# Kernel optimization log

Measured on AMD Instinct MI355X. Metric: run time of the kernel, lower is better.

## Reference

```python
import jax, jax.numpy as jnp
import numpy as np

D, H, W = 16, 16, 16          # token grid = img_size/patch_size at i_layer=0
NUM_HEADS = 8
DISTANCE = 10.0               # 10 - i_layer


def _local_pattern(d, h, w, distance):
    # faithful to local_nd_pattern: meshgrid (ij), flatten, cdist p=2, < distance
    g = jnp.meshgrid(jnp.arange(d), jnp.arange(h), jnp.arange(w), indexing='ij')
    coords = jnp.stack([c.reshape(-1) for c in g], axis=1).astype(jnp.float32)  # [N,3]
    diff = coords[:, None, :] - coords[None, :, :]                               # [N,N,3]
    dist = jnp.sqrt(jnp.sum(diff * diff, axis=-1))
    return dist < distance                                                       # [N,N] bool


def setup_inputs() -> dict:
    key = jax.random.key(0)
    k1, k2, k3 = jax.random.split(key, 3)
    dim = 256
    x = jax.random.normal(k1, (1, dim, D, H, W), dtype=jnp.float32)
    qkv_w = jax.random.normal(k2, (3 * dim, dim), dtype=jnp.float32) * (dim ** -0.5)
    proj_w = jax.random.normal(k3, (dim, dim), dtype=jnp.float32) * (dim ** -0.5)
    proj_b = jnp.zeros((dim,), dtype=jnp.float32)
    return {"x": x, "qkv_w": qkv_w, "proj_w": proj_w, "proj_b": proj_b}


def reference(x, qkv_w, proj_w, proj_b):
    b, c, d, h, w = x.shape
    n = d * h * w
    hd = c // NUM_HEADS
    mask = _local_pattern(d, h, w, DISTANCE)                  # [N,N] bool

    # b c d h w -> b (dhw) c
    tok = x.reshape(b, c, n).transpose(0, 2, 1)               # [B,N,C]
    qkv = jnp.einsum('bnc,oc->bno', tok, qkv_w)               # [B,N,3C]
    qkv = qkv.reshape(b, n, 3, NUM_HEADS, hd)
    qkv = qkv.transpose(2, 0, 3, 1, 4)                        # [3,B,H,N,hd]
    q, k, v = qkv[0], qkv[1], qkv[2]                          # [B,H,N,hd]

    scale = 1.0 / jnp.sqrt(jnp.asarray(hd, dtype=x.dtype))
    scores = jnp.einsum('bhnd,bhmd->bhnm', q, k) * scale      # [B,H,N,N]
    scores = jnp.where(mask[None, None], scores, -jnp.inf)
    attn = jax.nn.softmax(scores, axis=-1)
    out = jnp.einsum('bhnm,bhmd->bhnd', attn, v)              # [B,H,N,hd]

    out = out.transpose(0, 2, 1, 3).reshape(b, n, c)          # [B,N,C]
    out = jnp.einsum('bnc,oc->bno', out, proj_w) + proj_b
    # b (dhw) c -> b c d h w
    out = out.transpose(0, 2, 1).reshape(b, c, d, h, w)
    return out
```

## Files before the change

### kernel.cpp

```cpp
#include <hip/hip_runtime.h>
#include <hip/hip_bf16.h>

typedef __attribute__((ext_vector_type(8))) short short8;
typedef __attribute__((ext_vector_type(4))) float floatx4;

#define L2E 1.4426950408889634f

#if __has_builtin(__builtin_amdgcn_exp2f)
#define EXP2(x) __builtin_amdgcn_exp2f(x)
#else
#define EXP2(x) exp2f(x)
#endif
#if __has_builtin(__builtin_amdgcn_rcpf)
#define RCP(x) __builtin_amdgcn_rcpf(x)
#else
#define RCP(x) (1.0f / (x))
#endif

static __device__ __forceinline__ unsigned short f2bf(float f) {
    unsigned int u = __builtin_bit_cast(unsigned int, f);
    u += 0x7fffu + ((u >> 16) & 1u);
    return (unsigned short)(u >> 16);
}
static __device__ __forceinline__ unsigned int pk_bf16(float a, float b) {
    __hip_bfloat162 h2 = __float22bfloat162_rn(make_float2(a, b));
    unsigned int u;
    __builtin_memcpy(&u, &h2, 4);
    return u;
}

__global__ __launch_bounds__(256) void k_qkv(const float* __restrict__ x,
                                             const float* __restrict__ qw,
                                             unsigned short* __restrict__ qm,
                                             unsigned short* __restrict__ km,
                                             unsigned short* __restrict__ vt) {
    __shared__ __align__(16) unsigned short At[64][136];
    __shared__ __align__(16) unsigned short Wt[64][136];
    const int tid = threadIdx.x;
    const int wave = tid >> 6, lane = tid & 63;
    const int l16 = lane & 15, quad = lane >> 4;
    const int m0 = blockIdx.x * 64;
    const int o0 = blockIdx.y * 64;

    floatx4 acc[4] = {};
    for (int rnd = 0; rnd < 2; ++rnd) {
        const int cbase = rnd * 128;
        if (rnd) __syncthreads();
        {
            const int tok0 = (tid & 15) * 4;
            const int c0   = (tid >> 4) * 8;
            const float* xp = x + (size_t)(cbase + c0) * 4096 + m0 + tok0;
            float4 v[8];
            #pragma unroll
            for (int j = 0; j < 8; ++j)
                v[j] = *reinterpret_cast<const float4*>(xp + (size_t)j * 4096);
            #pragma unroll
            for (int t = 0; t < 4; ++t) {
                unsigned int d[4];
                d[0] = pk_bf16((&v[0].x)[t], (&v[1].x)[t]);
                d[1] = pk_bf16((&v[2].x)[t], (&v[3].x)[t]);
                d[2] = pk_bf16((&v[4].x)[t], (&v[5].x)[t]);
                d[3] = pk_bf16((&v[6].x)[t], (&v[7].x)[t]);
                __builtin_memcpy(&At[tok0 + t][c0], d, 16);
            }
        }
        {
            const int o_l = tid >> 2, cp = (tid & 3) * 32;
            const float4* wp = reinterpret_cast<const float4*>(
                qw + (size_t)(o0 + o_l) * 256 + cbase + cp);
            #pragma unroll
            for (int j = 0; j < 2; ++j) {
                const float4 g0 = wp[4 * j + 0], g1 = wp[4 * j + 1];
                const float4 g2 = wp[4 * j + 2], g3 = wp[4 * j + 3];
                unsigned int u[8];
                u[0] = pk_bf16(g0.x, g0.y); u[1] = pk_bf16(g0.z, g0.w);
                u[2] = pk_bf16(g1.x, g1.y); u[3] = pk_bf16(g1.z, g1.w);
                u[4] = pk_bf16(g2.x, g2.y); u[5] = pk_bf16(g2.z, g2.w);
                u[6] = pk_bf16(g3.x, g3.y); u[7] = pk_bf16(g3.z, g3.w);
                __builtin_memcpy(&Wt[o_l][cp + 16 * j], u, 32);
            }
        }
        __syncthreads();
        #pragma unroll
        for (int cc = 0; cc < 4; ++cc) {
            const int c0 = cc * 32 + quad * 8;
            const short8 a = *reinterpret_cast<const short8*>(&At[wave * 16 + l16][c0]);
            #pragma unroll
            for (int t4 = 0; t4 < 4; ++t4) {
                const short8 b = *reinterpret_cast<const short8*>(&Wt[t4 * 16 + l16][c0]);
                acc[t4] = __builtin_amdgcn_mfma_f32_16x16x32_bf16(a, b, acc[t4], 0, 0, 0);
            }
        }
    }

    const int s = o0 >> 8;
    if (s < 2) {
        const float qscale = 0.17677669529663687f * L2E;
        #pragma unroll
        for (int t4 = 0; t4 < 4; ++t4) {
            #pragma unroll
            for (int r = 0; r < 4; ++r) {
                const int n = m0 + wave * 16 + quad * 4 + r;
                const int o = o0 + t4 * 16 + l16;
                const int rem = o & 255, head = rem >> 5, t = rem & 31;
                if (s == 0)  qm[((size_t)head * 4096 + n) * 32 + t] = f2bf(acc[t4][r] * qscale);
                else         km[((size_t)head * 4096 + n) * 32 + t] = f2bf(acc[t4][r]);
            }
        }
    } else {
        __syncthreads();
        unsigned short (*Ct)[72] = reinterpret_cast<unsigned short(*)[72]>(&At[0][0]);
        #pragma unroll
        for (int t4 = 0; t4 < 4; ++t4) {
            unsigned int d2[2];
            d2[0] = pk_bf16(acc[t4][0], acc[t4][1]);
            d2[1] = pk_bf16(acc[t4][2], acc[t4][3]);
            __builtin_memcpy(&Ct[t4 * 16 + l16][wave * 16 + quad * 4], d2, 8);
        }
        __syncthreads();
        const int row = tid >> 2, col0 = (tid & 3) * 16;
        unsigned short* dst = vt + (size_t)(o0 - 512 + row) * 4096 + m0 + col0;
        const short8 ca = *reinterpret_cast<const short8*>(&Ct[row][col0]);
        const short8 cb = *reinterpret_cast<const short8*>(&Ct[row][col0 + 8]);
        *reinterpret_cast<short8*>(dst) = ca;
        *reinterpret_cast<short8*>(dst + 8) = cb;
    }
}

__global__ __launch_bounds__(256, 2) void k_attn(const unsigned short* __restrict__ qm,
                                                 const unsigned short* __restrict__ km,
                                                 const unsigned short* __restrict__ vt,
                                                 unsigned short* __restrict__ ao) {
    const int h   = blockIdx.y;
    const int nq0 = blockIdx.x * 64;
    const int tid = threadIdx.x;
    const int wv  = tid >> 6;
    const int lane = tid & 63;
    const int l16 = lane & 15, quad = lane >> 4;
    const int nqw = nq0 + wv * 16;

    __shared__ __align__(16) unsigned short Kt[2][2][2048];
    __shared__ __align__(16) unsigned short Vt[2][2][2048];
    __shared__ __align__(16) unsigned short PT[4][2][16][72];

    const short8 a_q = *reinterpret_cast<const short8*>(
        qm + ((size_t)h * 4096 + nqw + l16) * 32 + quad * 8);

    const int hq = (nqw >> 4) & 15;
    const int dq = nq0 >> 8;
    float dw2[4];
    #pragma unroll
    for (int r = 0; r < 4; ++r) {
        const float dw = (float)(quad * 4 + r - l16);
        dw2[r] = dw * dw;
    }

    const int dk_lo = (dq > 9) ? dq - 9 : 0;
    const int dk_hi = (dq < 6) ? dq + 9 : 15;
    const int NT = 4 * (dk_hi - dk_lo + 1);

    const int skey = tid >> 2;
    const int sdo  = (tid & 3) * 8;
    const int sdim = tid >> 3;
    const int skg  = tid & 7;
    const unsigned short* ksrc = km + ((size_t)h << 17) + skey * 32 + sdo;
    const unsigned short* vsrc = vt + (((size_t)h * 32 + sdim) << 12) + skg * 8;
    const int kdst = (skey * 32 + sdo) ^ ((skey & 7) << 3);
    const int vdst = (skg * 256 + sdim * 8) ^ (skg << 3);

    float l_acc = 0.f;
    floatx4 o_acc[2][2] = {};

#define J0T(T) (((dk_lo + ((T) >> 2)) << 8) + (((T) & 3) << 6))

    short8 rK[2], rV[2];
#define LOAD2(TA, TB) {                                                   \
        const int ja_ = J0T(TA), jb_ = J0T(TB);                           \
        rK[0] = *reinterpret_cast<const short8*>(ksrc + (size_t)ja_ * 32);\
        rV[0] = *reinterpret_cast<const short8*>(vsrc + ja_);             \
        rK[1] = *reinterpret_cast<const short8*>(ksrc + (size_t)jb_ * 32);\
        rV[1] = *reinterpret_cast<const short8*>(vsrc + jb_);             \
    }
#define WRITE2(NB) {                                                      \
        *reinterpret_cast<short8*>(&Kt[NB][0][kdst]) = rK[0];             \
        *reinterpret_cast<short8*>(&Vt[NB][0][vdst]) = rV[0];             \
        *reinterpret_cast<short8*>(&Kt[NB][1][kdst]) = rK[1];             \
        *reinterpret_cast<short8*>(&Vt[NB][1][vdst]) = rV[1];             \
    }

#define THR(T, TH) {                                                      \
        const int dk_ = dk_lo + ((T) >> 2), g_ = (T) & 3;                 \
        const int dd_ = dq - dk_;                                         \
        const int bb_ = 100 - dd_ * dd_;                                  \
        const int h0_ = hq - 4 * g_;                                      \
        TH[0] = bb_ - h0_ * h0_;                                          \
        TH[1] = bb_ - (h0_ - 1) * (h0_ - 1);                              \
        TH[2] = bb_ - (h0_ - 2) * (h0_ - 2);                              \
        TH[3] = bb_ - (h0_ - 3) * (h0_ - 3);                              \
    }

#define SSTAGE(TH, CB, SL) {                                              \
        _Pragma("unroll")                                                 \
        for (int t4 = 0; t4 < 4; ++t4) {                                  \
            const short8 kf = *reinterpret_cast<const short8*>(           \
                &Kt[CB][SL][((t4 * 16 + l16) * 32 + quad * 8) ^ ((l16 & 7) << 3)]); \
            const floatx4 sf = __builtin_amdgcn_mfma_f32_16x16x32_bf16(   \
                kf, a_q, (floatx4){0.f, 0.f, 0.f, 0.f}, 0, 0, 0);         \
            const float thrf = (float)TH[t4];                             \
            const float p0 = (dw2[0] < thrf) ? EXP2(sf[0]) : 0.f;         \
            const float p1 = (dw2[1] < thrf) ? EXP2(sf[1]) : 0.f;         \
            const float p2 = (dw2[2] < thrf) ? EXP2(sf[2]) : 0.f;         \
            const float p3 = (dw2[3] < thrf) ? EXP2(sf[3]) : 0.f;         \
            l_acc += (p0 + p1) + (p2 + p3);                               \
            unsigned int pair_[2];                                        \
            pair_[0] = pk_bf16(p0, p1);                                   \
            pair_[1] = pk_bf16(p2, p3);                                   \
            __builtin_memcpy(&PT[wv][SL][l16][t4 * 16 + quad * 4], pair_, 8); \
        }                                                                 \
    }

#define PVST(CB, SL) {                                                    \
        _Pragma("unroll")                                                 \
        for (int kt = 0; kt < 2; ++kt) {                                  \
            const short8 b_p = *reinterpret_cast<const short8*>(          \
                &PT[wv][SL][l16][kt * 32 + quad * 8]);                    \
            const int kg = kt * 4 + quad;                                 \
            _Pragma("unroll")                                             \
            for (int hf = 0; hf < 2; ++hf) {                              \
                const short8 vf = *reinterpret_cast<const short8*>(       \
                    &Vt[CB][SL][(kg * 256 + (hf * 16 + l16) * 8) ^ (kg << 3)]); \
                o_acc[SL][hf] = __builtin_amdgcn_mfma_f32_16x16x32_bf16(  \
                    vf, b_p, o_acc[SL][hf], 0, 0, 0);                     \
            }                                                             \
        }                                                                 \
    }

    LOAD2(0, 1)
    WRITE2(0)
    LOAD2(2, 3)
    __syncthreads();

    for (int t2 = 0; t2 < NT; t2 += 2) {
        const int cb = (t2 >> 1) & 1, nb = cb ^ 1;
        WRITE2(nb)
        {
            int ta = t2 + 4; if (ta >= NT) ta = NT - 1;
            int tb = t2 + 5; if (tb >= NT) tb = NT - 1;
            LOAD2(ta, tb)
        }
        int thA[4], thB[4];
        THR(t2, thA)
        THR(t2 + 1, thB)
        const bool liveA = (thA[0] > 0) | (thA[1] > 0) | (thA[2] > 0) | (thA[3] > 0);
        const bool liveB = (thB[0] > 0) | (thB[1] > 0) | (thB[2] > 0) | (thB[3] > 0);
        __builtin_amdgcn_s_setprio(1);
        if (liveA & liveB) {
            SSTAGE(thA, cb, 0)
            SSTAGE(thB, cb, 1)
            PVST(cb, 0)
            PVST(cb, 1)
        } else if (liveA) {
            SSTAGE(thA, cb, 0)
            PVST(cb, 0)
        } else if (liveB) {
            SSTAGE(thB, cb, 1)
            PVST(cb, 1)
        }
        __builtin_amdgcn_s_setprio(0);
        __syncthreads();
    }
#undef PVST
#undef SSTAGE
#undef THR
#undef WRITE2
#undef LOAD2
#undef J0T

    l_acc += __shfl_xor(l_acc, 16);
    l_acc += __shfl_xor(l_acc, 32);
    const float inv = RCP(l_acc);
    #pragma unroll
    for (int hf = 0; hf < 2; ++hf) {
        const floatx4 os = o_acc[0][hf] + o_acc[1][hf];
        unsigned int uu[2];
        uu[0] = pk_bf16(os[0] * inv, os[1] * inv);
        uu[1] = pk_bf16(os[2] * inv, os[3] * inv);
        __builtin_memcpy(ao + (size_t)(nqw + l16) * 256 + h * 32 + hf * 16 + quad * 4,
                         uu, 8);
    }
}

__global__ __launch_bounds__(256) void k_proj(const unsigned short* __restrict__ ao,
                                              const float* __restrict__ pw,
                                              const float* __restrict__ pb,
                                              float* __restrict__ out) {
    __shared__ __align__(16) unsigned short Pt[64][264];
    const int tid = threadIdx.x;
    const int wave = tid >> 6, lane = tid & 63;
    const int l16 = lane & 15, quad = lane >> 4;
    const int n0 = blockIdx.x * 32;
    const int m0 = blockIdx.y * 64;

    {
        const int o_l = tid >> 2, cp = (tid & 3) * 64;
        const float4* wp = reinterpret_cast<const float4*>(pw + (size_t)(m0 + o_l) * 256 + cp);
        #pragma unroll
        for (int j = 0; j < 4; ++j) {
            const float4 g0 = wp[4 * j + 0], g1 = wp[4 * j + 1];
            const float4 g2 = wp[4 * j + 2], g3 = wp[4 * j + 3];
            unsigned int u[8];
            u[0] = pk_bf16(g0.x, g0.y); u[1] = pk_bf16(g0.z, g0.w);
            u[2] = pk_bf16(g1.x, g1.y); u[3] = pk_bf16(g1.z, g1.w);
            u[4] = pk_bf16(g2.x, g2.y); u[5] = pk_bf16(g2.z, g2.w);
            u[6] = pk_bf16(g3.x, g3.y); u[7] = pk_bf16(g3.z, g3.w);
            __builtin_memcpy(&Pt[o_l][cp + 16 * j], u, 32);
        }
    }
    __syncthreads();

    floatx4 acc[2] = {};
    #pragma unroll
    for (int cc = 0; cc < 8; ++cc) {
        const int c0 = cc * 32 + quad * 8;
        const short8 a = *reinterpret_cast<const short8*>(&Pt[wave * 16 + l16][c0]);
        #pragma unroll
        for (int t4 = 0; t4 < 2; ++t4) {
            const short8 b = *reinterpret_cast<const short8*>(
                ao + (size_t)(n0 + t4 * 16 + l16) * 256 + c0);
            acc[t4] = __builtin_amdgcn_mfma_f32_16x16x32_bf16(a, b, acc[t4], 0, 0, 0);
        }
    }
    #pragma unroll
    for (int t4 = 0; t4 < 2; ++t4) {
        #pragma unroll
        for (int r = 0; r < 4; ++r) {
            const int o = m0 + wave * 16 + quad * 4 + r;
            const int n = n0 + t4 * 16 + l16;
            out[(size_t)o * 4096 + n] = acc[t4][r] + pb[o];
        }
    }
}

extern "C" void kernel_launch(void* const* d_in, const int* in_sizes, int n_in,
                              void* d_out, int out_size, void* d_ws, size_t ws_size,
                              hipStream_t stream) {
    const float* x      = (const float*)d_in[0];
    const float* qkv_w  = (const float*)d_in[1];
    const float* proj_w = (const float*)d_in[2];
    const float* proj_b = (const float*)d_in[3];
    float* out = (float*)d_out;

    char* B = (char*)d_ws;
    const size_t MB = 1u << 20;
    unsigned short* ao = (unsigned short*)(B);
    unsigned short* qm = (unsigned short*)(B + 2 * MB);
    unsigned short* km = (unsigned short*)(B + 4 * MB);
    unsigned short* vt = (unsigned short*)(B + 6 * MB);

    k_qkv<<<dim3(64, 12), 256, 0, stream>>>(x, qkv_w, qm, km, vt);
    k_attn<<<dim3(64, 8), 256, 0, stream>>>(qm, km, vt, ao);
    k_proj<<<dim3(128, 4), 256, 0, stream>>>(ao, proj_w, proj_b, out);
}
```

Measured before the change: 134.9 us.

## Split attention key range across two blocks and merge via atomics

Each query tile's key range is now split in half between two blocks, which doubles the attention grid to 1024 blocks so more of the GPU is occupied. Partial unnormalized outputs and row sums are accumulated with float atomics into an fp32 workspace that is zeroed by a memset, and normalization moves into the projection kernel. This relies on there being no running-max rescaling (fixed thresholds), so partial sums add directly. The cost is extra atomic traffic, a memset, and the projection reading fp32 instead of bf16.

```diff
diff --git a/kernel.cpp b/kernel.cpp
--- a/kernel.cpp
+++ b/kernel.cpp
@@ -130,9 +130,11 @@
 __global__ __launch_bounds__(256, 2) void k_attn(const unsigned short* __restrict__ qm,
                                                  const unsigned short* __restrict__ km,
                                                  const unsigned short* __restrict__ vt,
-                                                 unsigned short* __restrict__ ao) {
-    const int h   = blockIdx.y;
-    const int nq0 = blockIdx.x * 64;
+                                                 float* __restrict__ of32,
+                                                 float* __restrict__ lsum) {
+    const int h    = blockIdx.y;
+    const int half = blockIdx.x & 1;
+    const int nq0  = (blockIdx.x >> 1) * 64;
     const int tid = threadIdx.x;
     const int wv  = tid >> 6;
     const int lane = tid & 63;
@@ -157,7 +159,9 @@
 
     const int dk_lo = (dq > 9) ? dq - 9 : 0;
     const int dk_hi = (dq < 6) ? dq + 9 : 15;
-    const int NT = 4 * (dk_hi - dk_lo + 1);
+    const int NT  = 4 * (dk_hi - dk_lo + 1);
+    const int NTh = NT >> 1;
+    const int T0 = half * NTh, T1 = T0 + NTh;
 
     const int skey = tid >> 2;
     const int sdo  = (tid & 3) * 8;
@@ -235,17 +239,17 @@
         }                                                                 \
     }
 
-    LOAD2(0, 1)
+    LOAD2(T0, T0 + 1)
     WRITE2(0)
-    LOAD2(2, 3)
+    LOAD2(T0 + 2, T0 + 3)
     __syncthreads();
 
-    for (int t2 = 0; t2 < NT; t2 += 2) {
-        const int cb = (t2 >> 1) & 1, nb = cb ^ 1;
+    for (int t2 = T0; t2 < T1; t2 += 2) {
+        const int cb = ((t2 - T0) >> 1) & 1, nb = cb ^ 1;
         WRITE2(nb)
         {
-            int ta = t2 + 4; if (ta >= NT) ta = NT - 1;
-            int tb = t2 + 5; if (tb >= NT) tb = NT - 1;
+            int ta = t2 + 4; if (ta >= T1) ta = T1 - 1;
+            int tb = t2 + 5; if (tb >= T1) tb = T1 - 1;
             LOAD2(ta, tb)
         }
         int thA[4], thB[4];
@@ -278,19 +282,20 @@
 
     l_acc += __shfl_xor(l_acc, 16);
     l_acc += __shfl_xor(l_acc, 32);
-    const float inv = RCP(l_acc);
     #pragma unroll
     for (int hf = 0; hf < 2; ++hf) {
         const floatx4 os = o_acc[0][hf] + o_acc[1][hf];
-        unsigned int uu[2];
-        uu[0] = pk_bf16(os[0] * inv, os[1] * inv);
-        uu[1] = pk_bf16(os[2] * inv, os[3] * inv);
-        __builtin_memcpy(ao + (size_t)(nqw + l16) * 256 + h * 32 + hf * 16 + quad * 4,
-                         uu, 8);
-    }
-}
-
-__global__ __launch_bounds__(256) void k_proj(const unsigned short* __restrict__ ao,
+        float* op = of32 + (size_t)(nqw + l16) * 256 + h * 32 + hf * 16 + quad * 4;
+        unsafeAtomicAdd(op + 0, os[0]);
+        unsafeAtomicAdd(op + 1, os[1]);
+        unsafeAtomicAdd(op + 2, os[2]);
+        unsafeAtomicAdd(op + 3, os[3]);
+    }
+    if (lane < 16) unsafeAtomicAdd(lsum + (size_t)h * 4096 + nqw + l16, l_acc);
+}
+
+__global__ __launch_bounds__(256) void k_proj(const float* __restrict__ of32,
+                                              const float* __restrict__ lsum,
                                               const float* __restrict__ pw,
                                               const float* __restrict__ pb,
                                               float* __restrict__ out) {
@@ -325,8 +330,18 @@
         const short8 a = *reinterpret_cast<const short8*>(&Pt[wave * 16 + l16][c0]);
         #pragma unroll
         for (int t4 = 0; t4 < 2; ++t4) {
-            const short8 b = *reinterpret_cast<const short8*>(
-                ao + (size_t)(n0 + t4 * 16 + l16) * 256 + c0);
+            const int n = n0 + t4 * 16 + l16;
+            const float* op = of32 + (size_t)n * 256 + c0;
+            const float4 f0 = *reinterpret_cast<const float4*>(op);
+            const float4 f1 = *reinterpret_cast<const float4*>(op + 4);
+            const float inv = RCP(lsum[(size_t)cc * 4096 + n]);
+            unsigned int bw[4];
+            bw[0] = pk_bf16(f0.x * inv, f0.y * inv);
+            bw[1] = pk_bf16(f0.z * inv, f0.w * inv);
+            bw[2] = pk_bf16(f1.x * inv, f1.y * inv);
+            bw[3] = pk_bf16(f1.z * inv, f1.w * inv);
+            short8 b;
+            __builtin_memcpy(&b, bw, 16);
             acc[t4] = __builtin_amdgcn_mfma_f32_16x16x32_bf16(a, b, acc[t4], 0, 0, 0);
         }
     }
@@ -352,12 +367,14 @@
 
     char* B = (char*)d_ws;
     const size_t MB = 1u << 20;
-    unsigned short* ao = (unsigned short*)(B);
-    unsigned short* qm = (unsigned short*)(B + 2 * MB);
-    unsigned short* km = (unsigned short*)(B + 4 * MB);
-    unsigned short* vt = (unsigned short*)(B + 6 * MB);
-
+    float* of32 = (float*)(B);
+    float* lsum = (float*)(B + 4 * MB);
+    unsigned short* qm = (unsigned short*)(B + 5 * MB);
+    unsigned short* km = (unsigned short*)(B + 7 * MB);
+    unsigned short* vt = (unsigned short*)(B + 9 * MB);
+
+    hipMemsetAsync(B, 0, 4 * MB + 128 * 1024, stream);
     k_qkv<<<dim3(64, 12), 256, 0, stream>>>(x, qkv_w, qm, km, vt);
-    k_attn<<<dim3(64, 8), 256, 0, stream>>>(qm, km, vt, ao);
-    k_proj<<<dim3(128, 4), 256, 0, stream>>>(ao, proj_w, proj_b, out);
-}
+    k_attn<<<dim3(128, 8), 256, 0, stream>>>(qm, km, vt, of32, lsum);
+    k_proj<<<dim3(128, 4), 256, 0, stream>>>(of32, lsum, proj_w, proj_b, out);
+}
```

Result: slower. 145.4 us (+7.8%).
